# Kernel optimization log

Hardware: AMD Instinct MI355X
Metric: run time of the kernel (lower is better)

Reference implementation:

```python
import jax, jax.numpy as jnp
import numpy as np

ALPHA = 0.2          # LeakyReLU negative slope
NEG_INF = -9e15      # mask value from the torch source
N, F_IN, F_OUT = 8192, 128, 64


def setup_inputs() -> dict:
    key = jax.random.key(0)
    k1, k2, k3, k4, k5 = jax.random.split(key, 5)
    X = jax.random.normal(k1, (N, F_IN), dtype=jnp.float32)
    A = jax.random.randint(k2, (N, N), 0, 2, dtype=jnp.int32)  # 0/1 adjacency
    W = jax.random.normal(k3, (F_IN, F_OUT), dtype=jnp.float32) * 0.05
    a1 = jax.random.normal(k4, (F_OUT,), dtype=jnp.float32) * 0.05
    a2 = jax.random.normal(k5, (F_OUT,), dtype=jnp.float32) * 0.05
    return {"X": X, "A": A, "W": W, "a1": a1, "a2": a2}


def reference(X, A, W, a1, a2):
    # h = W(X)  (Linear, no bias)
    h = X @ W                                   # (N, F_out)
    # a([h_i || h_j]) == h_i @ a1 + h_j @ a2  (split of the 2F attention vector)
    s1 = h @ a1                                 # (N,)
    s2 = h @ a2                                 # (N,)
    e = jax.nn.leaky_relu(s1[:, None] + s2[None, :], ALPHA)  # (N, N)
    att = jnp.where(A > 0, e, NEG_INF)
    att = jax.nn.softmax(att, axis=1)           # row-wise masked softmax
    # dropout p=0.0 -> identity
    return att @ h                              # (N, F_out)
```

## Files before the change

kernel.cpp:

```cpp
#include <hip/hip_runtime.h>
#include <hip/hip_bf16.h>

#define NV 8192
#define FIN 128
#define FOUT 64

typedef __attribute__((ext_vector_type(8))) short short8;
typedef __attribute__((ext_vector_type(4))) float floatx4;

__device__ __forceinline__ uint f2bf_u(float f) {
  uint u = __float_as_uint(f);
  return (u + 0x7FFFu + ((u >> 16) & 1u)) >> 16;
}
__device__ __forceinline__ float bf2f(ushort b) {
  return __uint_as_float(((uint)b) << 16);
}

__global__ void k0_detect(const uint* __restrict__ X, int* __restrict__ flag) {
  const int lane = threadIdx.x & 63;
  uint u = X[lane];
  uint e = (u >> 7) & 0xFF;
  bool ok = (e >= 100u) && (e <= 135u);
  unsigned long long b = __ballot(ok);
  if (lane == 0) *flag = (__builtin_popcountll(b) >= 48) ? 1 : 0;
}

__global__ __launch_bounds__(256) void k1_proj(
    const void* __restrict__ Xv, const void* __restrict__ Wv,
    const void* __restrict__ a1v_, const void* __restrict__ a2v_,
    ushort* __restrict__ HtT, float* __restrict__ s1, float* __restrict__ s2,
    const int* __restrict__ flagp)
{
  const int is_bf16 = *flagp;
  const int wave = threadIdx.x >> 6;
  const int lane = threadIdx.x & 63;
  const int i0 = blockIdx.x * 64 + wave * 16;
  const int col = lane & 15;
  const int q   = lane >> 4;

  short8 bfrag[4][4];
  float a1f[4], a2f[4];
  if (is_bf16) {
    const ushort* W = (const ushort*)Wv;
#pragma unroll
    for (int nt = 0; nt < 4; ++nt)
#pragma unroll
      for (int kc = 0; kc < 4; ++kc) {
        short8 b;
#pragma unroll
        for (int j = 0; j < 8; ++j)
          b[j] = (short)W[(kc*32 + q*8 + j)*FOUT + nt*16 + col];
        bfrag[nt][kc] = b;
      }
#pragma unroll
    for (int nt = 0; nt < 4; ++nt) {
      a1f[nt] = bf2f(((const ushort*)a1v_)[nt*16 + col]);
      a2f[nt] = bf2f(((const ushort*)a2v_)[nt*16 + col]);
    }
  } else {
    const float* W = (const float*)Wv;
#pragma unroll
    for (int nt = 0; nt < 4; ++nt)
#pragma unroll
      for (int kc = 0; kc < 4; ++kc) {
        short8 b;
#pragma unroll
        for (int j = 0; j < 8; ++j)
          b[j] = (short)f2bf_u(W[(kc*32 + q*8 + j)*FOUT + nt*16 + col]);
        bfrag[nt][kc] = b;
      }
#pragma unroll
    for (int nt = 0; nt < 4; ++nt) {
      a1f[nt] = ((const float*)a1v_)[nt*16 + col];
      a2f[nt] = ((const float*)a2v_)[nt*16 + col];
    }
  }

  floatx4 acc[4] = {{0.f,0.f,0.f,0.f},{0.f,0.f,0.f,0.f},
                    {0.f,0.f,0.f,0.f},{0.f,0.f,0.f,0.f}};
#pragma unroll
  for (int kc = 0; kc < 4; ++kc) {
    short8 a;
    if (is_bf16) {
      a = *(const short8*)&((const ushort*)Xv)[(size_t)(i0 + col)*FIN + kc*32 + q*8];
    } else {
      const float* X = (const float*)Xv;
      float4 x0 = *(const float4*)&X[(size_t)(i0 + col)*FIN + kc*32 + q*8];
      float4 x1 = *(const float4*)&X[(size_t)(i0 + col)*FIN + kc*32 + q*8 + 4];
      a[0] = (short)f2bf_u(x0.x); a[1] = (short)f2bf_u(x0.y);
      a[2] = (short)f2bf_u(x0.z); a[3] = (short)f2bf_u(x0.w);
      a[4] = (short)f2bf_u(x1.x); a[5] = (short)f2bf_u(x1.y);
      a[6] = (short)f2bf_u(x1.z); a[7] = (short)f2bf_u(x1.w);
    }
#pragma unroll
    for (int nt = 0; nt < 4; ++nt)
      acc[nt] = __builtin_amdgcn_mfma_f32_16x16x32_bf16(a, bfrag[nt][kc], acc[nt], 0, 0, 0);
  }

  float s1p[4] = {0,0,0,0}, s2p[4] = {0,0,0,0};
#pragma unroll
  for (int nt = 0; nt < 4; ++nt) {
    ushort4 pk;
    pk.x = (ushort)f2bf_u(acc[nt][0]);
    pk.y = (ushort)f2bf_u(acc[nt][1]);
    pk.z = (ushort)f2bf_u(acc[nt][2]);
    pk.w = (ushort)f2bf_u(acc[nt][3]);
    *(ushort4*)&HtT[(size_t)(nt*16 + col)*NV + i0 + q*4] = pk;
#pragma unroll
    for (int reg = 0; reg < 4; ++reg) {
      s1p[reg] += acc[nt][reg] * a1f[nt];
      s2p[reg] += acc[nt][reg] * a2f[nt];
    }
  }
#pragma unroll
  for (int m = 1; m < 16; m <<= 1)
#pragma unroll
    for (int reg = 0; reg < 4; ++reg) {
      s1p[reg] += __shfl_xor(s1p[reg], m, 64);
      s2p[reg] += __shfl_xor(s2p[reg], m, 64);
    }
  if (col == 0)
#pragma unroll
    for (int reg = 0; reg < 4; ++reg) {
      s1[i0 + q*4 + reg] = s1p[reg];
      s2[i0 + q*4 + reg] = s2p[reg];
    }
}

#define CT 128
#define SLICES 4
#define SW (NV / SLICES)
#define NT (SW / CT)
#define PST 136

__global__ __launch_bounds__(256, 6) void k2_attn(
    const int* __restrict__ A, const ushort* __restrict__ HtT,
    const float* __restrict__ s1g, const float* __restrict__ s2g,
    float* __restrict__ Part, float* __restrict__ Lpart)
{
  __shared__ __align__(16) ushort Pl[16 * PST];
  __shared__ __align__(16) ushort Hl[64 * PST];

  const int tid  = threadIdx.x;
  const int wave = tid >> 6;
  const int lane = tid & 63;
  const int sl   = blockIdx.x & (SLICES - 1);
  const int rb   = blockIdx.x >> 2;
  const int i0   = rb * 16;
  const int q    = lane >> 4;
  const int mcol = lane & 15;
  const int r    = tid >> 4;
  const int cb   = (tid & 15) * 8;
  const int c0s  = sl * SW;
  const int t0   = (rb * 7) & (NT - 1);

  const float s1r = s1g[i0 + r];
  const size_t abase = (size_t)(i0 + r) * NV + c0s + cb;

  float Lp = 0.f;
  floatx4 acc = {0.f, 0.f, 0.f, 0.f};

  int4 av0, av1;
  float4 sv0, sv1;
  short8 hv[4];
  {
    const int c = t0 * CT;
    av0 = *(const int4*)&A[abase + c];
    av1 = *(const int4*)&A[abase + c + 4];
    sv0 = *(const float4*)&s2g[c0s + c + cb];
    sv1 = *(const float4*)&s2g[c0s + c + cb + 4];
#pragma unroll
    for (int it = 0; it < 4; ++it)
      hv[it] = *(const short8*)&HtT[(size_t)(r + 16*it) * NV + c0s + c + cb];
  }

  for (int t = 0; t < NT; ++t) {
    __syncthreads();

    {
      float x0 = s1r + sv0.x, x1 = s1r + sv0.y, x2 = s1r + sv0.z, x3 = s1r + sv0.w;
      float x4 = s1r + sv1.x, x5 = s1r + sv1.y, x6 = s1r + sv1.z, x7 = s1r + sv1.w;
      float w0 = av0.x ? __expf(fmaxf(x0, 0.2f*x0)) : 0.f;
      float w1 = av0.y ? __expf(fmaxf(x1, 0.2f*x1)) : 0.f;
      float w2 = av0.z ? __expf(fmaxf(x2, 0.2f*x2)) : 0.f;
      float w3 = av0.w ? __expf(fmaxf(x3, 0.2f*x3)) : 0.f;
      float w4 = av1.x ? __expf(fmaxf(x4, 0.2f*x4)) : 0.f;
      float w5 = av1.y ? __expf(fmaxf(x5, 0.2f*x5)) : 0.f;
      float w6 = av1.z ? __expf(fmaxf(x6, 0.2f*x6)) : 0.f;
      float w7 = av1.w ? __expf(fmaxf(x7, 0.2f*x7)) : 0.f;
      Lp += ((w0 + w1) + (w2 + w3)) + ((w4 + w5) + (w6 + w7));
      uint4 pk;
      pk.x = f2bf_u(w0) | (f2bf_u(w1) << 16);
      pk.y = f2bf_u(w2) | (f2bf_u(w3) << 16);
      pk.z = f2bf_u(w4) | (f2bf_u(w5) << 16);
      pk.w = f2bf_u(w6) | (f2bf_u(w7) << 16);
      *(uint4*)&Pl[r * PST + cb] = pk;
#pragma unroll
      for (int it = 0; it < 4; ++it)
        *(short8*)&Hl[(r + 16*it) * PST + cb] = hv[it];
    }

    __syncthreads();

    if (t + 1 < NT) {
      const int c2 = ((t + 1 + t0) & (NT - 1)) * CT;
      av0 = *(const int4*)&A[abase + c2];
      av1 = *(const int4*)&A[abase + c2 + 4];
      sv0 = *(const float4*)&s2g[c0s + c2 + cb];
      sv1 = *(const float4*)&s2g[c0s + c2 + cb + 4];
#pragma unroll
      for (int it = 0; it < 4; ++it)
        hv[it] = *(const short8*)&HtT[(size_t)(r + 16*it) * NV + c0s + c2 + cb];
    }

#pragma unroll
    for (int kc = 0; kc < 4; ++kc) {
      short8 af = *(const short8*)&Pl[mcol * PST + kc*32 + q*8];
      short8 bf = *(const short8*)&Hl[(wave*16 + mcol) * PST + kc*32 + q*8];
      acc = __builtin_amdgcn_mfma_f32_16x16x32_bf16(af, bf, acc, 0, 0, 0);
    }
  }

#pragma unroll
  for (int m = 1; m < 16; m <<= 1) Lp += __shfl_xor(Lp, m, 64);
  if (mcol == 0) Lpart[(size_t)sl * NV + i0 + r] = Lp;

#pragma unroll
  for (int reg = 0; reg < 4; ++reg) {
    int rr = q*4 + reg;
    Part[((size_t)sl * NV + i0 + rr) * FOUT + wave*16 + mcol] = acc[reg];
  }
}

__global__ __launch_bounds__(256) void k3_combine(
    const float* __restrict__ Part, const float* __restrict__ Lpart,
    void* __restrict__ outv, const int* __restrict__ flagp)
{
  const int is_bf16 = *flagp;
  const int g   = blockIdx.x * 256 + threadIdx.x;
  const int row = g >> 4;
  const int fb  = (g & 15) * 4;

  float4 s = {0.f, 0.f, 0.f, 0.f};
  float L = 0.f;
#pragma unroll
  for (int sl = 0; sl < SLICES; ++sl) {
    float4 v = *(const float4*)&Part[((size_t)sl * NV + row) * FOUT + fb];
    s.x += v.x; s.y += v.y; s.z += v.z; s.w += v.w;
    L += Lpart[(size_t)sl * NV + row];
  }
  const float inv = __frcp_rn(L);
  s.x *= inv; s.y *= inv; s.z *= inv; s.w *= inv;
  if (is_bf16) {
    ushort4 pk;
    pk.x = (ushort)f2bf_u(s.x); pk.y = (ushort)f2bf_u(s.y);
    pk.z = (ushort)f2bf_u(s.z); pk.w = (ushort)f2bf_u(s.w);
    *(ushort4*)&((ushort*)outv)[(size_t)row * FOUT + fb] = pk;
  } else {
    *(float4*)&((float*)outv)[(size_t)row * FOUT + fb] = s;
  }
}

extern "C" void kernel_launch(void* const* d_in, const int* in_sizes, int n_in,
                              void* d_out, int out_size, void* d_ws, size_t ws_size,
                              hipStream_t stream) {
  const void* X  = d_in[0];
  const int*  A  = (const int*)d_in[1];
  const void* W  = d_in[2];
  const void* a1 = d_in[3];
  const void* a2 = d_in[4];

  char* ws = (char*)d_ws;
  ushort* HtT   = (ushort*)ws;
  float*  s1    = (float*)(ws + (size_t)FOUT*NV*2);
  float*  s2    = s1 + NV;
  int*    flag  = (int*)(s2 + NV);
  float*  Part  = (float*)((char*)flag + 16);
  float*  Lpart = Part + (size_t)SLICES * NV * FOUT;

  hipLaunchKernelGGL(k0_detect, dim3(1), dim3(64), 0, stream,
                     (const uint*)X, flag);
  hipLaunchKernelGGL(k1_proj, dim3(NV/64), dim3(256), 0, stream,
                     X, W, a1, a2, HtT, s1, s2, flag);
  hipLaunchKernelGGL(k2_attn, dim3((NV/16) * SLICES), dim3(256), 0, stream,
                     A, HtT, s1, s2, Part, Lpart);
  hipLaunchKernelGGL(k3_combine, dim3(NV*FOUT/4/256), dim3(256), 0, stream,
                     Part, Lpart, d_out, flag);
}
```

Baseline: 381.0 us.

## Process 32 rows per attention block and halve column slices to reuse H tiles

```diff
diff --git a/kernel.cpp b/kernel.cpp
--- a/kernel.cpp
+++ b/kernel.cpp
@@ -128,45 +128,51 @@
 }
 
 #define CT 128
-#define SLICES 4
+#define SLICES 2
 #define SW (NV / SLICES)
-#define NT (SW / CT)
+#define NTL (SW / CT)
 #define PST 136
 
-__global__ __launch_bounds__(256, 6) void k2_attn(
+__global__ __launch_bounds__(256, 4) void k2_attn(
     const int* __restrict__ A, const ushort* __restrict__ HtT,
     const float* __restrict__ s1g, const float* __restrict__ s2g,
     float* __restrict__ Part, float* __restrict__ Lpart)
 {
-  __shared__ __align__(16) ushort Pl[16 * PST];
+  __shared__ __align__(16) ushort Pl[32 * PST];
   __shared__ __align__(16) ushort Hl[64 * PST];
+  __shared__ float Lrow[32];
 
   const int tid  = threadIdx.x;
   const int wave = tid >> 6;
   const int lane = tid & 63;
   const int sl   = blockIdx.x & (SLICES - 1);
-  const int rb   = blockIdx.x >> 2;
-  const int i0   = rb * 16;
+  const int rb   = blockIdx.x >> 1;
+  const int i0   = rb * 32;
   const int q    = lane >> 4;
   const int mcol = lane & 15;
   const int r    = tid >> 4;
   const int cb   = (tid & 15) * 8;
   const int c0s  = sl * SW;
-  const int t0   = (rb * 7) & (NT - 1);
-
-  const float s1r = s1g[i0 + r];
-  const size_t abase = (size_t)(i0 + r) * NV + c0s + cb;
-
-  float Lp = 0.f;
-  floatx4 acc = {0.f, 0.f, 0.f, 0.f};
-
-  int4 av0, av1;
+  const int t0   = (rb * 23) & (NTL - 1);
+
+  const float s1a = s1g[i0 + r];
+  const float s1b = s1g[i0 + r + 16];
+  const size_t abaseA = (size_t)(i0 + r) * NV + c0s + cb;
+  const size_t abaseB = (size_t)(i0 + r + 16) * NV + c0s + cb;
+
+  float LpA = 0.f, LpB = 0.f;
+  floatx4 acc0 = {0.f,0.f,0.f,0.f};
+  floatx4 acc1 = {0.f,0.f,0.f,0.f};
+
+  int4 avA0, avA1, avB0, avB1;
   float4 sv0, sv1;
   short8 hv[4];
   {
     const int c = t0 * CT;
-    av0 = *(const int4*)&A[abase + c];
-    av1 = *(const int4*)&A[abase + c + 4];
+    avA0 = *(const int4*)&A[abaseA + c];
+    avA1 = *(const int4*)&A[abaseA + c + 4];
+    avB0 = *(const int4*)&A[abaseB + c];
+    avB1 = *(const int4*)&A[abaseB + c + 4];
     sv0 = *(const float4*)&s2g[c0s + c + cb];
     sv1 = *(const float4*)&s2g[c0s + c + cb + 4];
 #pragma unroll
@@ -174,27 +180,46 @@
       hv[it] = *(const short8*)&HtT[(size_t)(r + 16*it) * NV + c0s + c + cb];
   }
 
-  for (int t = 0; t < NT; ++t) {
+  for (int t = 0; t < NTL; ++t) {
     __syncthreads();
 
     {
-      float x0 = s1r + sv0.x, x1 = s1r + sv0.y, x2 = s1r + sv0.z, x3 = s1r + sv0.w;
-      float x4 = s1r + sv1.x, x5 = s1r + sv1.y, x6 = s1r + sv1.z, x7 = s1r + sv1.w;
-      float w0 = av0.x ? __expf(fmaxf(x0, 0.2f*x0)) : 0.f;
-      float w1 = av0.y ? __expf(fmaxf(x1, 0.2f*x1)) : 0.f;
-      float w2 = av0.z ? __expf(fmaxf(x2, 0.2f*x2)) : 0.f;
-      float w3 = av0.w ? __expf(fmaxf(x3, 0.2f*x3)) : 0.f;
-      float w4 = av1.x ? __expf(fmaxf(x4, 0.2f*x4)) : 0.f;
-      float w5 = av1.y ? __expf(fmaxf(x5, 0.2f*x5)) : 0.f;
-      float w6 = av1.z ? __expf(fmaxf(x6, 0.2f*x6)) : 0.f;
-      float w7 = av1.w ? __expf(fmaxf(x7, 0.2f*x7)) : 0.f;
-      Lp += ((w0 + w1) + (w2 + w3)) + ((w4 + w5) + (w6 + w7));
+      float x0 = s1a + sv0.x, x1 = s1a + sv0.y, x2 = s1a + sv0.z, x3 = s1a + sv0.w;
+      float x4 = s1a + sv1.x, x5 = s1a + sv1.y, x6 = s1a + sv1.z, x7 = s1a + sv1.w;
+      float w0 = avA0.x ? __expf(fmaxf(x0, 0.2f*x0)) : 0.f;
+      float w1 = avA0.y ? __expf(fmaxf(x1, 0.2f*x1)) : 0.f;
+      float w2 = avA0.z ? __expf(fmaxf(x2, 0.2f*x2)) : 0.f;
+      float w3 = avA0.w ? __expf(fmaxf(x3, 0.2f*x3)) : 0.f;
+      float w4 = avA1.x ? __expf(fmaxf(x4, 0.2f*x4)) : 0.f;
+      float w5 = avA1.y ? __expf(fmaxf(x5, 0.2f*x5)) : 0.f;
+      float w6 = avA1.z ? __expf(fmaxf(x6, 0.2f*x6)) : 0.f;
+      float w7 = avA1.w ? __expf(fmaxf(x7, 0.2f*x7)) : 0.f;
+      LpA += ((w0 + w1) + (w2 + w3)) + ((w4 + w5) + (w6 + w7));
       uint4 pk;
       pk.x = f2bf_u(w0) | (f2bf_u(w1) << 16);
       pk.y = f2bf_u(w2) | (f2bf_u(w3) << 16);
       pk.z = f2bf_u(w4) | (f2bf_u(w5) << 16);
       pk.w = f2bf_u(w6) | (f2bf_u(w7) << 16);
       *(uint4*)&Pl[r * PST + cb] = pk;
+
+      float y0 = s1b + sv0.x, y1 = s1b + sv0.y, y2 = s1b + sv0.z, y3 = s1b + sv0.w;
+      float y4 = s1b + sv1.x, y5 = s1b + sv1.y, y6 = s1b + sv1.z, y7 = s1b + sv1.w;
+      float v0 = avB0.x ? __expf(fmaxf(y0, 0.2f*y0)) : 0.f;
+      float v1 = avB0.y ? __expf(fmaxf(y1, 0.2f*y1)) : 0.f;
+      float v2 = avB0.z ? __expf(fmaxf(y2, 0.2f*y2)) : 0.f;
+      float v3 = avB0.w ? __expf(fmaxf(y3, 0.2f*y3)) : 0.f;
+      float v4 = avB1.x ? __expf(fmaxf(y4, 0.2f*y4)) : 0.f;
+      float v5 = avB1.y ? __expf(fmaxf(y5, 0.2f*y5)) : 0.f;
+      float v6 = avB1.z ? __expf(fmaxf(y6, 0.2f*y6)) : 0.f;
+      float v7 = avB1.w ? __expf(fmaxf(y7, 0.2f*y7)) : 0.f;
+      LpB += ((v0 + v1) + (v2 + v3)) + ((v4 + v5) + (v6 + v7));
+      uint4 pk2;
+      pk2.x = f2bf_u(v0) | (f2bf_u(v1) << 16);
+      pk2.y = f2bf_u(v2) | (f2bf_u(v3) << 16);
+      pk2.z = f2bf_u(v4) | (f2bf_u(v5) << 16);
+      pk2.w = f2bf_u(v6) | (f2bf_u(v7) << 16);
+      *(uint4*)&Pl[(r + 16) * PST + cb] = pk2;
+
 #pragma unroll
       for (int it = 0; it < 4; ++it)
         *(short8*)&Hl[(r + 16*it) * PST + cb] = hv[it];
@@ -202,10 +227,12 @@
 
     __syncthreads();
 
-    if (t + 1 < NT) {
-      const int c2 = ((t + 1 + t0) & (NT - 1)) * CT;
-      av0 = *(const int4*)&A[abase + c2];
-      av1 = *(const int4*)&A[abase + c2 + 4];
+    if (t + 1 < NTL) {
+      const int c2 = ((t + 1 + t0) & (NTL - 1)) * CT;
+      avA0 = *(const int4*)&A[abaseA + c2];
+      avA1 = *(const int4*)&A[abaseA + c2 + 4];
+      avB0 = *(const int4*)&A[abaseB + c2];
+      avB1 = *(const int4*)&A[abaseB + c2 + 4];
       sv0 = *(const float4*)&s2g[c0s + c2 + cb];
       sv1 = *(const float4*)&s2g[c0s + c2 + cb + 4];
 #pragma unroll
@@ -215,21 +242,32 @@
 
 #pragma unroll
     for (int kc = 0; kc < 4; ++kc) {
-      short8 af = *(const short8*)&Pl[mcol * PST + kc*32 + q*8];
       short8 bf = *(const short8*)&Hl[(wave*16 + mcol) * PST + kc*32 + q*8];
-      acc = __builtin_amdgcn_mfma_f32_16x16x32_bf16(af, bf, acc, 0, 0, 0);
-    }
-  }
-
-#pragma unroll
-  for (int m = 1; m < 16; m <<= 1) Lp += __shfl_xor(Lp, m, 64);
-  if (mcol == 0) Lpart[(size_t)sl * NV + i0 + r] = Lp;
+      short8 af0 = *(const short8*)&Pl[mcol * PST + kc*32 + q*8];
+      short8 af1 = *(const short8*)&Pl[(16 + mcol) * PST + kc*32 + q*8];
+      acc0 = __builtin_amdgcn_mfma_f32_16x16x32_bf16(af0, bf, acc0, 0, 0, 0);
+      acc1 = __builtin_amdgcn_mfma_f32_16x16x32_bf16(af1, bf, acc1, 0, 0, 0);
+    }
+  }
+
+#pragma unroll
+  for (int m = 1; m < 16; m <<= 1) {
+    LpA += __shfl_xor(LpA, m, 64);
+    LpB += __shfl_xor(LpB, m, 64);
+  }
+  if (mcol == 0) { Lrow[r] = LpA; Lrow[r + 16] = LpB; }
+  __syncthreads();
 
 #pragma unroll
   for (int reg = 0; reg < 4; ++reg) {
-    int rr = q*4 + reg;
-    Part[((size_t)sl * NV + i0 + rr) * FOUT + wave*16 + mcol] = acc[reg];
-  }
+    int r0 = q*4 + reg;
+    Part[((size_t)sl * NV + i0 + r0) * FOUT + wave*16 + mcol] = acc0[reg];
+    Part[((size_t)sl * NV + i0 + 16 + r0) * FOUT + wave*16 + mcol] = acc1[reg];
+  }
+  if (tid < 32 && lane < 32) {  }
+  if (mcol == 0 && wave == 0) {
+  }
+  if (tid < 32) Lpart[(size_t)sl * NV + i0 + tid] = Lrow[tid];
 }
 
 __global__ __launch_bounds__(256) void k3_combine(
@@ -282,7 +320,7 @@
                      (const uint*)X, flag);
   hipLaunchKernelGGL(k1_proj, dim3(NV/64), dim3(256), 0, stream,
                      X, W, a1, a2, HtT, s1, s2, flag);
-  hipLaunchKernelGGL(k2_attn, dim3((NV/16) * SLICES), dim3(256), 0, stream,
+  hipLaunchKernelGGL(k2_attn, dim3((NV/32) * SLICES), dim3(256), 0, stream,
                      A, HtT, s1, s2, Part, Lpart);
   hipLaunchKernelGGL(k3_combine, dim3(NV*FOUT/4/256), dim3(256), 0, stream,
                      Part, Lpart, d_out, flag);
```

After: 370.3 us. -2.8%, faster.
